# Performance work log

Measured on AMD Instinct MI355X. Metric: run time of the kernel, lower is better.

Reference implementation:

```python
import jax, jax.numpy as jnp
import numpy as np

B, C = 2, 8
SPATIAL = (128, 128, 128)


def setup_inputs() -> dict:
    key = jax.random.key(0)
    k1, k2 = jax.random.split(key)
    pred = jax.random.normal(k1, (B, C) + SPATIAL, dtype=jnp.float32)
    ref = jax.random.randint(k2, (B, 1) + SPATIAL, 0, C, dtype=jnp.int32)
    return {"pred": pred, "ref": ref}


def reference(pred, ref):
    # Hard Dice, exclude_background=True (background index 0), weighted=False,
    # labels = range(nb_class), reduction='mean'.
    b, c = pred.shape[0], pred.shape[1]
    pred_lbl = jnp.argmax(pred, axis=1).reshape(b, -1)   # (B, S) int labels
    ref_lbl = ref.reshape(b, -1)                          # (B, S) int labels

    classes = jnp.arange(1, c, dtype=pred_lbl.dtype)      # skip background (index 0)
    # (B, C-1, S) boolean one-vs-all masks; single pass over the volume per tensor.
    p1 = pred_lbl[:, None, :] == classes[None, :, None]
    r1 = ref_lbl[:, None, :] == classes[None, :, None]

    inter = jnp.sum(p1 & r1, axis=-1).astype(jnp.float32)  # (B, C-1)
    psum = jnp.sum(p1, axis=-1).astype(jnp.float32)
    rsum = jnp.sum(r1, axis=-1).astype(jnp.float32)

    hasref = rsum > 0                                      # (B, C-1)
    union = psum + rsum
    # torch: loss1 = 2*inter/union then masked_fill_(~hasref, 0)
    dice = jnp.where(hasref, 2.0 * inter / jnp.where(union > 0, union, 1.0), 0.0)

    sumweights = jnp.sum(hasref.astype(jnp.float32), axis=1)  # (B,)
    loss = jnp.sum(dice, axis=1) / sumweights                 # (B,)
    return jnp.mean(loss)                                     # reduction='mean'
```

## Files before the change

kernel.cpp:

```cpp
#include <hip/hip_runtime.h>


#define S_VOX (128 * 128 * 128)
#define S4    (S_VOX / 4)
#define NC    8
#define NFG   7

#define WS_INTS (2 * 3 * NFG)

#define PROC_COMP(C)                                                     \
    {                                                                    \
        float bv = a0.C; int bi = 0;                                     \
        if (a1.C > bv) { bv = a1.C; bi = 1; }                            \
        if (a2.C > bv) { bv = a2.C; bi = 2; }                            \
        if (a3.C > bv) { bv = a3.C; bi = 3; }                            \
        if (a4.C > bv) { bv = a4.C; bi = 4; }                            \
        if (a5.C > bv) { bv = a5.C; bi = 5; }                            \
        if (a6.C > bv) { bv = a6.C; bi = 6; }                            \
        if (a7.C > bv) { bv = a7.C; bi = 7; }                            \
        const int rr = r.C;                                              \
        _Pragma("unroll")                                                \
        for (int c = 1; c < NC; ++c) {                                   \
            cp[c - 1] += (bi == c);                                      \
            cr[c - 1] += (rr == c);                                      \
            ci[c - 1] += (int)((bi == c) & (rr == c));                   \
        }                                                                \
    }

__global__ __launch_bounds__(256) void dice_count_kernel(
    const float4* __restrict__ pred4, const int4* __restrict__ ref4,
    int* __restrict__ ws)
{
    const int b = blockIdx.y;
    int ci[NFG], cp[NFG], cr[NFG];
#pragma unroll
    for (int k = 0; k < NFG; ++k) { ci[k] = 0; cp[k] = 0; cr[k] = 0; }

    const int tid      = blockIdx.x * blockDim.x + threadIdx.x;
    const int nthreads = gridDim.x * blockDim.x;
    const long long predBase = (long long)b * NC * S4;
    const long long refBase  = (long long)b * S4;

    for (int g = tid; g < S4; g += nthreads) {
        const float4 a0 = pred4[predBase + (long long)0 * S4 + g];
        const float4 a1 = pred4[predBase + (long long)1 * S4 + g];
        const float4 a2 = pred4[predBase + (long long)2 * S4 + g];
        const float4 a3 = pred4[predBase + (long long)3 * S4 + g];
        const float4 a4 = pred4[predBase + (long long)4 * S4 + g];
        const float4 a5 = pred4[predBase + (long long)5 * S4 + g];
        const float4 a6 = pred4[predBase + (long long)6 * S4 + g];
        const float4 a7 = pred4[predBase + (long long)7 * S4 + g];
        const int4   r  = ref4[refBase + g];
        PROC_COMP(x)
        PROC_COMP(y)
        PROC_COMP(z)
        PROC_COMP(w)
    }

#pragma unroll
    for (int k = 0; k < NFG; ++k) {
#pragma unroll
        for (int off = 32; off > 0; off >>= 1) {
            ci[k] += __shfl_down(ci[k], off, 64);
            cp[k] += __shfl_down(cp[k], off, 64);
            cr[k] += __shfl_down(cr[k], off, 64);
        }
    }

    __shared__ int sh[3 * NFG];
    if (threadIdx.x < 3 * NFG) sh[threadIdx.x] = 0;
    __syncthreads();

    const int lane = threadIdx.x & 63;
    if (lane == 0) {
#pragma unroll
        for (int k = 0; k < NFG; ++k) {
            atomicAdd(&sh[k], ci[k]);
            atomicAdd(&sh[NFG + k], cp[k]);
            atomicAdd(&sh[2 * NFG + k], cr[k]);
        }
    }
    __syncthreads();

    if (threadIdx.x < 3 * NFG) {
        atomicAdd(&ws[b * (3 * NFG) + threadIdx.x], sh[threadIdx.x]);
    }
}

__global__ void dice_finalize_kernel(const int* __restrict__ ws,
                                     float* __restrict__ out)
{
    if (blockIdx.x == 0 && threadIdx.x == 0) {
        float total = 0.0f;
#pragma unroll
        for (int b = 0; b < 2; ++b) {
            const int* w = ws + b * (3 * NFG);
            float sumd = 0.0f, sumw = 0.0f;
#pragma unroll
            for (int k = 0; k < NFG; ++k) {
                const int I = w[k];
                const int P = w[NFG + k];
                const int R = w[2 * NFG + k];
                if (R > 0) {
                    sumw += 1.0f;
                    sumd += 2.0f * (float)I / (float)(P + R);
                }
            }
            total += sumd / sumw;
        }
        out[0] = 0.5f * total;
    }
}

extern "C" void kernel_launch(void* const* d_in, const int* in_sizes, int n_in,
                              void* d_out, int out_size, void* d_ws, size_t ws_size,
                              hipStream_t stream) {
    const float* pred = (const float*)d_in[0];
    const int*   ref  = (const int*)d_in[1];
    float*       out  = (float*)d_out;
    int*         ws   = (int*)d_ws;

    hipMemsetAsync(ws, 0, WS_INTS * sizeof(int), stream);

    dim3 grid(256, 2, 1);
    dim3 block(256, 1, 1);
    dice_count_kernel<<<grid, block, 0, stream>>>(
        (const float4*)pred, (const int4*)ref, ws);
    dice_finalize_kernel<<<1, 64, 0, stream>>>(ws, out);
}
```

Baseline: 209.8 us.

## Pack per-class counters into byte lanes of 64-bit words and double grid

```diff
diff --git a/kernel.cpp b/kernel.cpp
--- a/kernel.cpp
+++ b/kernel.cpp
@@ -4,9 +4,10 @@
 #define S_VOX (128 * 128 * 128)
 #define S4    (S_VOX / 4)
 #define NC    8
-#define NFG   7
 
-#define WS_INTS (2 * 3 * NFG)
+#define WS_INTS (2 * 3 * NC)
+
+#define BYTE_MASK 0x00FF00FF00FF00FFULL
 
 #define PROC_COMP(C)                                                     \
     {                                                                    \
@@ -19,12 +20,10 @@
         if (a6.C > bv) { bv = a6.C; bi = 6; }                            \
         if (a7.C > bv) { bv = a7.C; bi = 7; }                            \
         const int rr = r.C;                                              \
-        _Pragma("unroll")                                                \
-        for (int c = 1; c < NC; ++c) {                                   \
-            cp[c - 1] += (bi == c);                                      \
-            cr[c - 1] += (rr == c);                                      \
-            ci[c - 1] += (int)((bi == c) & (rr == c));                   \
-        }                                                                \
+        const unsigned long long pa = 1ULL << (bi * 8);                  \
+        pcnt += pa;                                                      \
+        rcnt += 1ULL << (rr * 8);                                        \
+        icnt += (bi == rr) ? pa : 0ULL;                                  \
     }
 
 __global__ __launch_bounds__(256) void dice_count_kernel(
@@ -32,9 +31,7 @@
     int* __restrict__ ws)
 {
     const int b = blockIdx.y;
-    int ci[NFG], cp[NFG], cr[NFG];
-#pragma unroll
-    for (int k = 0; k < NFG; ++k) { ci[k] = 0; cp[k] = 0; cr[k] = 0; }
+    unsigned long long icnt = 0, pcnt = 0, rcnt = 0;
 
     const int tid      = blockIdx.x * blockDim.x + threadIdx.x;
     const int nthreads = gridDim.x * blockDim.x;
@@ -57,33 +54,42 @@
         PROC_COMP(w)
     }
 
-#pragma unroll
-    for (int k = 0; k < NFG; ++k) {
-#pragma unroll
-        for (int off = 32; off > 0; off >>= 1) {
-            ci[k] += __shfl_down(ci[k], off, 64);
-            cp[k] += __shfl_down(cp[k], off, 64);
-            cr[k] += __shfl_down(cr[k], off, 64);
-        }
+    unsigned w[12];
+    {
+        const unsigned long long li = icnt & BYTE_MASK, hi = (icnt >> 8) & BYTE_MASK;
+        const unsigned long long lp = pcnt & BYTE_MASK, hp = (pcnt >> 8) & BYTE_MASK;
+        const unsigned long long lr = rcnt & BYTE_MASK, hr = (rcnt >> 8) & BYTE_MASK;
+        w[0] = (unsigned)li; w[1] = (unsigned)(li >> 32); w[2]  = (unsigned)hi; w[3]  = (unsigned)(hi >> 32);
+        w[4] = (unsigned)lp; w[5] = (unsigned)(lp >> 32); w[6]  = (unsigned)hp; w[7]  = (unsigned)(hp >> 32);
+        w[8] = (unsigned)lr; w[9] = (unsigned)(lr >> 32); w[10] = (unsigned)hr; w[11] = (unsigned)(hr >> 32);
     }
 
-    __shared__ int sh[3 * NFG];
-    if (threadIdx.x < 3 * NFG) sh[threadIdx.x] = 0;
+#pragma unroll
+    for (int j = 0; j < 12; ++j) {
+#pragma unroll
+        for (int off = 32; off > 0; off >>= 1)
+            w[j] += __shfl_down(w[j], off, 64);
+    }
+
+    __shared__ unsigned sh[12];
+    if (threadIdx.x < 12) sh[threadIdx.x] = 0;
     __syncthreads();
 
-    const int lane = threadIdx.x & 63;
-    if (lane == 0) {
+    if ((threadIdx.x & 63) == 0) {
 #pragma unroll
-        for (int k = 0; k < NFG; ++k) {
-            atomicAdd(&sh[k], ci[k]);
-            atomicAdd(&sh[NFG + k], cp[k]);
-            atomicAdd(&sh[2 * NFG + k], cr[k]);
-        }
+        for (int j = 0; j < 12; ++j) atomicAdd(&sh[j], w[j]);
     }
     __syncthreads();
 
-    if (threadIdx.x < 3 * NFG) {
-        atomicAdd(&ws[b * (3 * NFG) + threadIdx.x], sh[threadIdx.x]);
+    if (threadIdx.x < 12) {
+        const int j = threadIdx.x;
+        const int t = j >> 2;
+        const int q = j & 3;
+        const int c0tab[4] = {0, 4, 1, 5};
+        const int c0 = c0tab[q];
+        const unsigned v = sh[j];
+        atomicAdd(&ws[b * 24 + t * 8 + c0],     (int)(v & 0xFFFFu));
+        atomicAdd(&ws[b * 24 + t * 8 + c0 + 2], (int)(v >> 16));
     }
 }
 
@@ -94,13 +100,13 @@
         float total = 0.0f;
 #pragma unroll
         for (int b = 0; b < 2; ++b) {
-            const int* w = ws + b * (3 * NFG);
+            const int* w = ws + b * 24;
             float sumd = 0.0f, sumw = 0.0f;
 #pragma unroll
-            for (int k = 0; k < NFG; ++k) {
-                const int I = w[k];
-                const int P = w[NFG + k];
-                const int R = w[2 * NFG + k];
+            for (int c = 1; c < NC; ++c) {
+                const int I = w[0 * 8 + c];
+                const int P = w[1 * 8 + c];
+                const int R = w[2 * 8 + c];
                 if (R > 0) {
                     sumw += 1.0f;
                     sumd += 2.0f * (float)I / (float)(P + R);
@@ -122,7 +128,7 @@
 
     hipMemsetAsync(ws, 0, WS_INTS * sizeof(int), stream);
 
-    dim3 grid(256, 2, 1);
+    dim3 grid(512, 2, 1);
     dim3 block(256, 1, 1);
     dice_count_kernel<<<grid, block, 0, stream>>>(
         (const float4*)pred, (const int4*)ref, ws);
```

New measurement: 213.1 us. No clear change (+1.6%).
